# Kernel tuning notes

Measured on AMD Instinct MI355X. Metric: run time of the kernel, lower is better.

The kernel has to match this reference:

```python
import jax, jax.numpy as jnp
import numpy as np

D = 1024
POOL_SIZES = [1024, 512, 256, 128, 64]  # n_pos=32*32 -> n_codes=64
CODEBOOK_SIZE = 512
BATCH = 32
W_SCALE = 0.03125  # ~1/sqrt(D) so pre-softmax logits stay O(1)


def setup_inputs() -> dict:
    key = jax.random.key(0)
    ks = jax.random.split(key, 7)
    x = jax.random.normal(ks[0], (BATCH, POOL_SIZES[0], D), dtype=jnp.float32)
    queries = jax.random.normal(ks[1], (len(POOL_SIZES), POOL_SIZES[0], D), dtype=jnp.float32)
    wq = jax.random.normal(ks[2], (len(POOL_SIZES), D, D), dtype=jnp.float32) * W_SCALE
    wk = jax.random.normal(ks[3], (len(POOL_SIZES), D, D), dtype=jnp.float32) * W_SCALE
    wv = jax.random.normal(ks[4], (len(POOL_SIZES), D, D), dtype=jnp.float32) * W_SCALE
    wo = jax.random.normal(ks[5], (len(POOL_SIZES), D, D), dtype=jnp.float32) * W_SCALE
    codebook = jax.random.normal(ks[6], (CODEBOOK_SIZE, D), dtype=jnp.float32)
    return {"x": x, "queries": queries, "wq": wq, "wk": wk, "wv": wv, "wo": wo, "codebook": codebook}


def reference(x, queries, wq, wk, wv, wo, codebook):
    # StackedPooling: S -> 1024 -> 512 -> 256 -> 128 -> 64 via AttentionPool stages
    scale = D ** (-0.5)
    h = x
    for i, K in enumerate(POOL_SIZES):
        q = queries[i, :K, :] @ wq[i]              # [K, D] learned queries, q_proj
        k = jnp.einsum("bsd,de->bse", h, wk[i])    # [B, S, D]
        v = jnp.einsum("bsd,de->bse", h, wv[i])    # [B, S, D]
        logits = jnp.einsum("kd,bsd->bks", q, k) * scale
        attn = jax.nn.softmax(logits, axis=-1)     # [B, K, S]
        pooled = jnp.einsum("bks,bsd->bkd", attn, v)
        h = jnp.einsum("bkd,de->bke", pooled, wo[i])  # [B, K, D]
    # VQ codebook quantization: nearest code per latent (squared L2)
    z = h                                          # [B, n_codes, D]
    d2 = (jnp.sum(z * z, axis=-1, keepdims=True)
          - 2.0 * jnp.einsum("bkd,cd->bkc", z, codebook)
          + jnp.sum(codebook * codebook, axis=-1))  # [B, n_codes, C]
    idx = jnp.argmin(d2, axis=-1)                  # [B, n_codes] int
    z_q = codebook[idx]                            # [B, n_codes, D]
    # straight-through estimator
    out = z + jax.lax.stop_gradient(z_q - z)
    return out
```

## Files before the change

### kernel.cpp

```cpp
#include <hip/hip_runtime.h>


#define MB (1024ull * 1024ull)

typedef unsigned short u16;
typedef __attribute__((ext_vector_type(4))) float f32x4;
typedef __bf16 bf16x8 __attribute__((ext_vector_type(8)));

__device__ __forceinline__ u16 f2bf(float f) {
  unsigned u = __float_as_uint(f);
  unsigned r = u + 0x7FFFu + ((u >> 16) & 1u);
  return (u16)(r >> 16);
}
__device__ __forceinline__ float bf2f(u16 h) {
  return __uint_as_float(((unsigned)h) << 16);
}

typedef __attribute__((address_space(1))) const void GASV;
typedef __attribute__((address_space(3))) void LASV;
__device__ __forceinline__ void async16(const void* g, void* l) {
  __builtin_amdgcn_global_load_lds((GASV*)g, (LASV*)l, 16, 0, 0);
}

__device__ __forceinline__ int xcd_swz(int bid, int nwg) {
  const int q8 = nwg >> 3, r8 = nwg & 7;
  const int xcd = bid & 7, idx = bid >> 3;
  return (xcd < r8 ? xcd * (q8 + 1) : r8 * (q8 + 1) + (xcd - r8) * q8) + idx;
}

template<int MODE>
__global__ __launch_bounds__(512, 1)
void gemm_c(const u16* __restrict__ A, const u16* __restrict__ B,
            float* __restrict__ Cf, u16* __restrict__ Cb,
            int M, int N, int KLEN, int ld,
            long long sA, long long sB, long long sC, int ldc, float alpha,
            int nxt, int nyt)
{
  __shared__ u16 lds[65536];
  const int tid  = threadIdx.x;
  const int lane = tid & 63;
  const int w    = tid >> 6;
  const int wr   = w >> 2, wc = w & 3;

  const int wg = xcd_swz((int)blockIdx.x, (int)gridDim.x);
  const int bx = wg % nxt;
  const int by = (wg / nxt) % nyt;
  const int bz = wg / (nxt * nyt);

  const int m0 = by * 256, n0 = bx * 256;
  const u16* Ab = A + (size_t)bz * sA;
  const u16* Bb = B + (size_t)bz * sB;
  const int NT = KLEN >> 6;

  f32x4 acc[8][4] = {};

  const int Rl  = tid >> 2;
  const int sgs = (tid & 3) ^ ((tid >> 3) & 3);
  int ra0 = m0 + Rl;        ra0 = ra0 < M - 1 ? ra0 : M - 1;
  int ra1 = m0 + 128 + Rl;  ra1 = ra1 < M - 1 ? ra1 : M - 1;
  int rb0 = n0 + Rl;        rb0 = rb0 < N - 1 ? rb0 : N - 1;
  int rb1 = n0 + 128 + Rl;  rb1 = rb1 < N - 1 ? rb1 : N - 1;
  const u16* gA0 = Ab + (size_t)ra0 * ld + (sgs << 3);
  const u16* gA1 = Ab + (size_t)ra1 * ld + (sgs << 3);
  const u16* gB0 = Bb + (size_t)rb0 * ld + (sgs << 3);
  const u16* gB1 = Bb + (size_t)rb1 * ld + (sgs << 3);
  const int ldst = (w << 4) * 32;

  auto stageH = [&](int mat, int buf, int kh, int tile) {
    const int tt = tile < NT ? tile : NT - 1;
    const int kc = (tt << 6) + (kh << 5);
    u16* d = &lds[(mat << 15) + (buf << 14) + (kh << 13) + ldst];
    if (mat == 0) { async16(gA0 + kc, d); async16(gA1 + kc, d + 4096); }
    else          { async16(gB0 + kc, d); async16(gB1 + kc, d + 4096); }
  };

  const int rsel = lane & 15;
  const int ksub = lane >> 4;
  const int sw   = ksub ^ ((rsel >> 1) & 3);
  const u16* ldsA = &lds[(wr * 128 + rsel) * 32 + sw * 8];
  const u16* ldsB = &lds[32768 + (wc * 64 + rsel) * 32 + sw * 8];

  auto phase = [&](int buf, int kh, int mh, bf16x8* b,
                   int smat, int sbuf, int skh, int stile, int vm) {
    bf16x8 a[4];
    if (mh == 0) {
#pragma unroll
      for (int ni = 0; ni < 4; ++ni)
        b[ni] = *(const bf16x8*)&ldsB[buf * 16384 + kh * 8192 + ni * 512];
    }
#pragma unroll
    for (int mi = 0; mi < 4; ++mi)
      a[mi] = *(const bf16x8*)&ldsA[buf * 16384 + kh * 8192 + mh * 2048 + mi * 512];
    stageH(smat, sbuf, skh, stile);
    if (vm == 10)     asm volatile("s_waitcnt vmcnt(10)" ::: "memory");
    else if (vm == 6) asm volatile("s_waitcnt vmcnt(6)" ::: "memory");
    __builtin_amdgcn_s_barrier();
    asm volatile("s_waitcnt lgkmcnt(0)" ::: "memory");
    __builtin_amdgcn_sched_barrier(0);
    __builtin_amdgcn_s_setprio(1);
#pragma unroll
    for (int mi = 0; mi < 4; ++mi)
#pragma unroll
      for (int ni = 0; ni < 4; ++ni)
        acc[mh * 4 + mi][ni] = __builtin_amdgcn_mfma_f32_16x16x32_bf16(
            a[mi], b[ni], acc[mh * 4 + mi][ni], 0, 0, 0);
    __builtin_amdgcn_s_setprio(0);
    __builtin_amdgcn_s_barrier();
  };

  stageH(1, 0, 0, 0); stageH(0, 0, 0, 0); stageH(1, 0, 1, 0); stageH(0, 0, 1, 0);
  stageH(1, 1, 0, 1); stageH(0, 1, 0, 1); stageH(1, 1, 1, 1);
  asm volatile("s_waitcnt vmcnt(6)" ::: "memory");
  __builtin_amdgcn_s_barrier();

  const int NI = NT >> 1;
  for (int it = 0; it < NI; ++it) {
    const int t0 = it << 1, t1 = t0 + 1;
    bf16x8 b0[4], b1[4];
    phase(0, 0, 0, b0, 0, 1, 1, t1,     -1);
    phase(0, 0, 1, b0, 1, 0, 0, t0 + 2, -1);
    phase(0, 1, 0, b1, 0, 0, 0, t0 + 2, -1);
    phase(0, 1, 1, b1, 1, 0, 1, t0 + 2, 10);
    phase(1, 0, 0, b0, 0, 0, 1, t0 + 2, -1);
    phase(1, 0, 1, b0, 1, 1, 0, t1 + 2, 10);
    phase(1, 1, 0, b1, 0, 1, 0, t1 + 2, -1);
    phase(1, 1, 1, b1, 1, 1, 1, t1 + 2, 6);
  }
  asm volatile("s_waitcnt vmcnt(0)" ::: "memory");

#pragma unroll
  for (int mi = 0; mi < 8; ++mi)
#pragma unroll
    for (int ni = 0; ni < 4; ++ni)
#pragma unroll
      for (int i = 0; i < 4; ++i) {
        const int row = m0 + wr * 128 + mi * 16 + ((lane >> 4) << 2) + i;
        const int col = n0 + wc * 64 + ni * 16 + rsel;
        if (row < M && col < N) {
          const float v = acc[mi][ni][i] * alpha;
          const size_t off = (size_t)bz * sC + (size_t)row * ldc + col;
          if (MODE == 0) Cf[off] = v;
          else           Cb[off] = f2bf(v);
        }
      }
}

template<int MODE>
__global__ __launch_bounds__(256, 2)
void gemm_s(const u16* __restrict__ A, const u16* __restrict__ B,
            float* __restrict__ Cf, u16* __restrict__ Cb,
            int M, int N, int KLEN, int ld,
            long long sA, long long sB, long long sC, int ldc, float alpha,
            int nxt, int nyt)
{
  __shared__ u16 lds[32768];
  const int tid  = threadIdx.x;
  const int lane = tid & 63;
  const int w    = tid >> 6;
  const int wr   = w >> 1, wc = w & 1;

  const int wg = xcd_swz((int)blockIdx.x, (int)gridDim.x);
  const int bx = wg % nxt;
  const int by = (wg / nxt) % nyt;
  const int bz = wg / (nxt * nyt);

  const int m0 = by * 128, n0 = bx * 128;
  const u16* Ab = A + (size_t)bz * sA;
  const u16* Bb = B + (size_t)bz * sB;
  const int NT = KLEN >> 6;

  f32x4 acc[4][4] = {};

  const int Rl  = tid >> 3;
  const int sgs = (tid & 7) ^ (Rl & 7);
  const int ldst = (w << 3) * 64;

  auto stage = [&](int t, int buf) {
    const int kc = t << 6;
#pragma unroll
    for (int mat = 0; mat < 2; ++mat)
#pragma unroll
      for (int j = 0; j < 4; ++j) {
        int rg = (mat ? n0 : m0) + j * 32 + Rl;
        const int lim = (mat ? N : M) - 1;
        rg = rg < lim ? rg : lim;
        const u16* src = (mat ? Bb : Ab) + (size_t)rg * ld + kc + (sgs << 3);
        async16(src, &lds[(buf << 14) + (mat << 13) + j * 2048 + ldst]);
      }
  };

  const int rsel = lane & 15, ksub = lane >> 4;
  const int e  = rsel & 7;
  const int s0 = ((e >> 2) << 2) | (ksub ^ (e & 3));
  const int s1 = s0 ^ 4;
  const u16* ldsA0 = &lds[(wr * 64 + rsel) * 64 + s0 * 8];
  const u16* ldsA1 = &lds[(wr * 64 + rsel) * 64 + s1 * 8];
  const u16* ldsB0 = &lds[8192 + (wc * 64 + rsel) * 64 + s0 * 8];
  const u16* ldsB1 = &lds[8192 + (wc * 64 + rsel) * 64 + s1 * 8];

  stage(0, 0);
  for (int t = 0; t < NT; ++t) {
    const int buf = t & 1;
    if (t + 1 < NT) {
      stage(t + 1, buf ^ 1);
      asm volatile("s_waitcnt vmcnt(8)" ::: "memory");
    } else {
      asm volatile("s_waitcnt vmcnt(0)" ::: "memory");
    }
    __builtin_amdgcn_s_barrier();
    bf16x8 af[4][2], bf[4][2];
#pragma unroll
    for (int f = 0; f < 4; ++f) {
      af[f][0] = *(const bf16x8*)&ldsA0[buf * 16384 + f * 1024];
      af[f][1] = *(const bf16x8*)&ldsA1[buf * 16384 + f * 1024];
      bf[f][0] = *(const bf16x8*)&ldsB0[buf * 16384 + f * 1024];
      bf[f][1] = *(const bf16x8*)&ldsB1[buf * 16384 + f * 1024];
    }
    asm volatile("s_waitcnt lgkmcnt(0)" ::: "memory");
    __builtin_amdgcn_sched_barrier(0);
    __builtin_amdgcn_s_setprio(1);
#pragma unroll
    for (int mi = 0; mi < 4; ++mi)
#pragma unroll
      for (int ni = 0; ni < 4; ++ni)
#pragma unroll
        for (int kh = 0; kh < 2; ++kh)
          acc[mi][ni] = __builtin_amdgcn_mfma_f32_16x16x32_bf16(
              af[mi][kh], bf[ni][kh], acc[mi][ni], 0, 0, 0);
    __builtin_amdgcn_s_setprio(0);
    __builtin_amdgcn_s_barrier();
  }

#pragma unroll
  for (int mi = 0; mi < 4; ++mi)
#pragma unroll
    for (int ni = 0; ni < 4; ++ni)
#pragma unroll
      for (int i = 0; i < 4; ++i) {
        const int row = m0 + wr * 64 + mi * 16 + ((lane >> 4) << 2) + i;
        const int col = n0 + wc * 64 + ni * 16 + rsel;
        if (row < M && col < N) {
          const float v = acc[mi][ni][i] * alpha;
          const size_t off = (size_t)bz * sC + (size_t)row * ldc + col;
          if (MODE == 0) Cf[off] = v;
          else           Cb[off] = f2bf(v);
        }
      }
}

__global__ void cast_k(const float* __restrict__ in, u16* __restrict__ out,
                       long long n4)
{
  long long i = (long long)blockIdx.x * 256 + threadIdx.x;
  const long long stride = (long long)gridDim.x * 256;
  for (; i < n4; i += stride) {
    const float4 v = *(const float4*)&in[i << 2];
    *(ushort4*)&out[i << 2] = make_ushort4(f2bf(v.x), f2bf(v.y), f2bf(v.z), f2bf(v.w));
  }
}

__global__ __launch_bounds__(256)
void cast_trans_k(const float* __restrict__ in, u16* __restrict__ h,
                  u16* __restrict__ ht)
{
  __shared__ float t[32][33];
  const int z = blockIdx.z;
  const float* src = in + (size_t)z * 1048576;
  u16* dh = h  + (size_t)z * 1048576;
  u16* dt = ht + (size_t)z * 1048576;
  const int x0 = blockIdx.x * 32, y0 = blockIdx.y * 32;
  const int tx = threadIdx.x, ty = threadIdx.y;
#pragma unroll
  for (int k = 0; k < 4; ++k) {
    const float v = src[(size_t)(y0 + ty + 8 * k) * 1024 + (x0 + tx)];
    t[ty + 8 * k][tx] = v;
    dh[(size_t)(y0 + ty + 8 * k) * 1024 + (x0 + tx)] = f2bf(v);
  }
  __syncthreads();
#pragma unroll
  for (int k = 0; k < 4; ++k)
    dt[(size_t)(x0 + ty + 8 * k) * 1024 + (y0 + tx)] = f2bf(t[tx][ty + 8 * k]);
}

__global__ __launch_bounds__(256)
void transpose_cast_k(const float* __restrict__ in, u16* __restrict__ out)
{
  __shared__ float t[32][33];
  const int z = blockIdx.z;
  const float* src = in + (size_t)z * 1048576;
  u16* dst = out + (size_t)z * 1048576;
  const int x0 = blockIdx.x * 32, y0 = blockIdx.y * 32;
  const int tx = threadIdx.x, ty = threadIdx.y;
#pragma unroll
  for (int k = 0; k < 4; ++k)
    t[ty + 8 * k][tx] = src[(size_t)(y0 + ty + 8 * k) * 1024 + (x0 + tx)];
  __syncthreads();
#pragma unroll
  for (int k = 0; k < 4; ++k)
    dst[(size_t)(x0 + ty + 8 * k) * 1024 + (y0 + tx)] = f2bf(t[tx][ty + 8 * k]);
}

__global__ __launch_bounds__(256)
void transpose_u16_k(const u16* __restrict__ in, u16* __restrict__ out, int R)
{
  __shared__ u16 t[32][33];
  const size_t zi = (size_t)blockIdx.z * R * 1024;
  const size_t zo = (size_t)blockIdx.z * 1024 * R;
  const int x0 = blockIdx.x * 32, y0 = blockIdx.y * 32;
  const int tx = threadIdx.x, ty = threadIdx.y;
#pragma unroll
  for (int k = 0; k < 4; ++k)
    t[ty + 8 * k][tx] = in[zi + (size_t)(y0 + ty + 8 * k) * 1024 + (x0 + tx)];
  __syncthreads();
#pragma unroll
  for (int k = 0; k < 4; ++k)
    out[zo + (size_t)(x0 + ty + 8 * k) * R + (y0 + tx)] = t[tx][ty + 8 * k];
}

__global__ __launch_bounds__(256)
void softmax_b(const u16* __restrict__ lg, u16* __restrict__ at, int S)
{
  const size_t row = blockIdx.x;
  const u16* src = lg + row * S;
  const int tid = threadIdx.x;
  float v[4];
  float mx = -3.402823466e38f;
#pragma unroll
  for (int c = 0; c < 4; ++c) {
    const int j = tid + c * 256;
    v[c] = (j < S) ? bf2f(src[j]) : -3.402823466e38f;
    mx = fmaxf(mx, v[c]);
  }
#pragma unroll
  for (int o = 32; o > 0; o >>= 1) mx = fmaxf(mx, __shfl_xor(mx, o));
  __shared__ float rmx[4];
  if ((tid & 63) == 0) rmx[tid >> 6] = mx;
  __syncthreads();
  mx = fmaxf(fmaxf(rmx[0], rmx[1]), fmaxf(rmx[2], rmx[3]));
  float sum = 0.f;
#pragma unroll
  for (int c = 0; c < 4; ++c) { v[c] = expf(v[c] - mx); sum += v[c]; }
#pragma unroll
  for (int o = 32; o > 0; o >>= 1) sum += __shfl_xor(sum, o);
  __shared__ float rsm[4];
  if ((tid & 63) == 0) rsm[tid >> 6] = sum;
  __syncthreads();
  sum = rsm[0] + rsm[1] + rsm[2] + rsm[3];
  const float inv = 1.0f / sum;
  u16* dst = at + row * S;
#pragma unroll
  for (int c = 0; c < 4; ++c) {
    const int j = tid + c * 256;
    if (j < S) dst[j] = f2bf(v[c] * inv);
  }
}

__global__ __launch_bounds__(256)
void cnorm_kernel(const float* __restrict__ cb, float* __restrict__ cn)
{
  const int c = blockIdx.x;
  const float4 v = ((const float4*)(cb + (size_t)c * 1024))[threadIdx.x];
  float s = v.x * v.x + v.y * v.y + v.z * v.z + v.w * v.w;
#pragma unroll
  for (int o = 32; o > 0; o >>= 1) s += __shfl_xor(s, o);
  __shared__ float r4[4];
  if ((threadIdx.x & 63) == 0) r4[threadIdx.x >> 6] = s;
  __syncthreads();
  if (threadIdx.x == 0) cn[c] = r4[0] + r4[1] + r4[2] + r4[3];
}

__global__ __launch_bounds__(256)
void argmin_gather_k(const float* __restrict__ dot, const float* __restrict__ cn,
                     const float* __restrict__ cb, float* __restrict__ out)
{
  const size_t lat = blockIdx.x;
  const int tid = threadIdx.x;
  const float* dr = dot + lat * 512;
  float best = 3.402823466e38f;
  int bi = 0;
#pragma unroll
  for (int cc = 0; cc < 2; ++cc) {
    const int c = tid + cc * 256;
    const float sc = cn[c] - 2.0f * dr[c];
    if (sc < best || (sc == best && c < bi)) { best = sc; bi = c; }
  }
  __shared__ float rb[256];
  __shared__ int   ri[256];
  rb[tid] = best; ri[tid] = bi;
  __syncthreads();
  for (int s = 128; s > 0; s >>= 1) {
    if (tid < s) {
      const float ob = rb[tid + s];
      const int oi = ri[tid + s];
      if (ob < rb[tid] || (ob == rb[tid] && oi < ri[tid])) { rb[tid] = ob; ri[tid] = oi; }
    }
    __syncthreads();
  }
  const int sel = ri[0];
  ((float4*)(out + lat * 1024))[tid] = ((const float4*)(cb + (size_t)sel * 1024))[tid];
}

__global__ void fill_kernel(float* p, float v, int n) {
  const int i = blockIdx.x * 256 + threadIdx.x;
  if (i < n) p[i] = v;
}

static void gX(hipStream_t st, int mode, int force,
               const u16* A, const u16* B, float* Cf, u16* Cb,
               int M, int N, int KLEN, int ld,
               long long sA, long long sB, long long sC, int ldc,
               int batch, float alpha)
{
  const int b256 = ((M + 255) / 256) * ((N + 255) / 256) * batch;
  const bool big = (force == 2) || (force == 0 && b256 >= 192 && (KLEN & 127) == 0);
  if (big) {
    const int nxt = (N + 255) / 256, nyt = (M + 255) / 256;
    dim3 grid(nxt * nyt * batch), blk(512);
    if (mode == 0)
      gemm_c<0><<<grid, blk, 0, st>>>(A, B, Cf, Cb, M, N, KLEN, ld, sA, sB, sC, ldc, alpha, nxt, nyt);
    else
      gemm_c<1><<<grid, blk, 0, st>>>(A, B, Cf, Cb, M, N, KLEN, ld, sA, sB, sC, ldc, alpha, nxt, nyt);
  } else {
    const int nxt = (N + 127) / 128, nyt = (M + 127) / 128;
    dim3 grid(nxt * nyt * batch), blk(256);
    if (mode == 0)
      gemm_s<0><<<grid, blk, 0, st>>>(A, B, Cf, Cb, M, N, KLEN, ld, sA, sB, sC, ldc, alpha, nxt, nyt);
    else
      gemm_s<1><<<grid, blk, 0, st>>>(A, B, Cf, Cb, M, N, KLEN, ld, sA, sB, sC, ldc, alpha, nxt, nyt);
  }
}

extern "C" void kernel_launch(void* const* d_in, const int* in_sizes, int n_in,
                              void* d_out, int out_size, void* d_ws, size_t ws_size,
                              hipStream_t stream)
{
  const float* x   = (const float*)d_in[0];
  const float* qry = (const float*)d_in[1];
  const float* wq  = (const float*)d_in[2];
  const float* wk  = (const float*)d_in[3];
  const float* wv  = (const float*)d_in[4];
  const float* wo  = (const float*)d_in[5];
  const float* cb  = (const float*)d_in[6];
  float* out = (float*)d_out;

  const size_t NEED = 312 * MB;
  if (ws_size < NEED) {
    fill_kernel<<<(out_size + 255) / 256, 256, 0, stream>>>(out, (float)ws_size, out_size);
    return;
  }
  char* ws = (char*)d_ws;
  const long long W = 1048576;
  u16*  QKb  = (u16*)(ws + 0 * MB);
  u16*  WVOb = (u16*)(ws + 10 * MB);
  u16*  WVOs = (u16*)(ws + 20 * MB);
  u16*  CBb  = (u16*)(ws + 30 * MB);
  float* CN  = (float*)(ws + 31 * MB);
  u16*  QKP  = (u16*)(ws + 32 * MB);
  u16*  WCb  = (u16*)(ws + 40 * MB);
  u16*  WC5  = (u16*)(ws + 48 * MB);
  u16*  CBW  = (u16*)(ws + 50 * MB);
  float* DOT = (float*)(ws + 51 * MB);
  u16*  U    = (u16*)(ws + 56 * MB);
  u16*  UT   = (u16*)(ws + 120 * MB);
  u16*  ATb  = (u16*)(ws + 184 * MB);
  u16*  LOG  = (u16*)(ws + 248 * MB);
  u16*  QSb   = (u16*)(ws + 56 * MB);
  u16*  WQb   = (u16*)(ws + 66 * MB);
  u16*  WKb   = (u16*)(ws + 76 * MB);
  u16*  WVb   = (u16*)(ws + 86 * MB);
  u16*  WOTb  = (u16*)(ws + 96 * MB);
  u16*  WqkTb = (u16*)(ws + 106 * MB);

  const int S_in[5]  = {1024, 1024, 512, 256, 128};
  const int K_out[5] = {1024, 512, 256, 128, 64};

  cast_k<<<2048, 256, 0, stream>>>(qry, QSb, 1310720ll);
  cast_k<<<2048, 256, 0, stream>>>(wq, WQb, 1310720ll);
  cast_k<<<2048, 256, 0, stream>>>(wk, WKb, 1310720ll);
  cast_k<<<2048, 256, 0, stream>>>(wv, WVb, 1310720ll);
  cast_k<<<512, 256, 0, stream>>>(cb, CBb, 131072ll);
  dim3 tb(32, 8), tg5(32, 32, 5);
  transpose_cast_k<<<tg5, tb, 0, stream>>>(wo, WOTb);
  cnorm_kernel<<<512, 256, 0, stream>>>(cb, CN);

  gX(stream, 1, 0, WKb, WQb, nullptr, WqkTb, 1024, 1024, 1024, 1024, W, W, W, 1024, 5, 1.0f);
  gX(stream, 1, 0, QSb, WqkTb, nullptr, QKb, 1024, 1024, 1024, 1024, W, W, W, 1024, 5, 1.0f);
  gX(stream, 1, 0, WOTb, WVb, nullptr, WVOb, 1024, 1024, 1024, 1024, W, W, W, 1024, 5, 1.0f);
  gX(stream, 1, 0, WVb, WOTb, nullptr, WVOs, 1024, 1024, 1024, 1024, W, W, W, 1024, 5, 1.0f);

  hipMemcpyAsync(WCb, WVOs, 2 * MB, hipMemcpyDeviceToDevice, stream);
  gX(stream, 1, 0, WCb,         WVOb + 1 * W, nullptr, WCb + 1 * W, 1024, 1024, 1024, 1024, 0, 0, 0, 1024, 1, 1.0f);
  gX(stream, 1, 0, WCb + 1 * W, WVOb + 2 * W, nullptr, WCb + 2 * W, 1024, 1024, 1024, 1024, 0, 0, 0, 1024, 1, 1.0f);
  gX(stream, 1, 0, WCb + 2 * W, WVOb + 3 * W, nullptr, WCb + 3 * W, 1024, 1024, 1024, 1024, 0, 0, 0, 1024, 1, 1.0f);
  gX(stream, 1, 0, WCb + 3 * W, WVOb + 4 * W, nullptr, WC5,         1024, 1024, 1024, 1024, 0, 0, 0, 1024, 1, 1.0f);
  gX(stream, 1, 0, QKb + W, WCb, nullptr, QKP, 1024, 1024, 1024, 1024, W, W, W, 1024, 4, 1.0f);
  gX(stream, 1, 0, CBb, WC5, nullptr, CBW, 512, 1024, 1024, 1024, 0, 0, 0, 1024, 1, 1.0f);

  dim3 tgx(32, 32, 32);
  cast_trans_k<<<tgx, tb, 0, stream>>>(x, U, UT);

  for (int i = 0; i < 5; ++i) {
    const int S = S_in[i], KO = K_out[i];
    const u16* qk = (i == 0) ? QKb : QKP + (size_t)(i - 1) * W;

    gX(stream, 1, (i == 0) ? 1 : 0, qk, U, nullptr, LOG,
       KO, S, 1024, 1024, 0, (long long)S * 1024, (long long)KO * S, S, 32, 0.03125f);
    softmax_b<<<32 * KO, 256, 0, stream>>>(LOG, ATb, S);
    gX(stream, 1, (i == 0) ? 2 : 0, ATb, UT, nullptr, U,
       KO, 1024, S, S, (long long)KO * S, (long long)1024 * S, (long long)KO * 1024, 1024, 32, 1.0f);
    if (i < 4) {
      dim3 tgt(32, KO / 32, 32);
      transpose_u16_k<<<tgt, tb, 0, stream>>>(U, UT, KO);
    }
  }

  gX(stream, 0, 0, U, CBW, DOT, nullptr,
     2048, 512, 1024, 1024, 0, 0, 0, 512, 1, 1.0f);
  argmin_gather_k<<<2048, 256, 0, stream>>>(DOT, CN, cb, out);
}
```

Before: 733.1 us.

## Fuse transposed output into GEMM epilogue, merge cast kernels, batch weight products

Adds a GEMM mode that writes a transposed bf16 copy of the pooled output from the epilogue, replacing the separate transpose kernel between stages. The transposed buffer ping-pongs between two workspace regions. The five cast launches are merged into one kernel. The WK·WQ and WV·WOT products now run as a single batch of 10, and the memcpy is replaced by a transpose. The forced big/small GEMM tile selection is dropped. The transposed epilogue stores are strided and uncoalesced, which may cost more than the transpose kernel they replace.

```diff
diff --git a/kernel.cpp b/kernel.cpp
--- a/kernel.cpp
+++ b/kernel.cpp
@@ -31,10 +31,10 @@
 template<int MODE>
 __global__ __launch_bounds__(512, 1)
 void gemm_c(const u16* __restrict__ A, const u16* __restrict__ B,
-            float* __restrict__ Cf, u16* __restrict__ Cb,
+            float* __restrict__ Cf, u16* __restrict__ Cb, u16* __restrict__ Ct,
             int M, int N, int KLEN, int ld,
-            long long sA, long long sB, long long sC, int ldc, float alpha,
-            int nxt, int nyt)
+            long long sA, long long sB, long long sC, int ldc,
+            long long sT, int ldt, float alpha, int nxt, int nyt)
 {
   __shared__ u16 lds[65536];
   const int tid  = threadIdx.x;
@@ -140,7 +140,12 @@
           const float v = acc[mi][ni][i] * alpha;
           const size_t off = (size_t)bz * sC + (size_t)row * ldc + col;
           if (MODE == 0) Cf[off] = v;
-          else           Cb[off] = f2bf(v);
+          else {
+            const u16 h = f2bf(v);
+            Cb[off] = h;
+            if (MODE == 2)
+              Ct[(size_t)bz * sT + (size_t)col * ldt + row] = h;
+          }
         }
       }
 }
@@ -148,10 +153,10 @@
 template<int MODE>
 __global__ __launch_bounds__(256, 2)
 void gemm_s(const u16* __restrict__ A, const u16* __restrict__ B,
-            float* __restrict__ Cf, u16* __restrict__ Cb,
+            float* __restrict__ Cf, u16* __restrict__ Cb, u16* __restrict__ Ct,
             int M, int N, int KLEN, int ld,
-            long long sA, long long sB, long long sC, int ldc, float alpha,
-            int nxt, int nyt)
+            long long sA, long long sB, long long sC, int ldc,
+            long long sT, int ldt, float alpha, int nxt, int nyt)
 {
   __shared__ u16 lds[32768];
   const int tid  = threadIdx.x;
@@ -243,19 +248,34 @@
           const float v = acc[mi][ni][i] * alpha;
           const size_t off = (size_t)bz * sC + (size_t)row * ldc + col;
           if (MODE == 0) Cf[off] = v;
-          else           Cb[off] = f2bf(v);
+          else {
+            const u16 h = f2bf(v);
+            Cb[off] = h;
+            if (MODE == 2)
+              Ct[(size_t)bz * sT + (size_t)col * ldt + row] = h;
+          }
         }
       }
 }
 
-__global__ void cast_k(const float* __restrict__ in, u16* __restrict__ out,
-                       long long n4)
+__global__ void multicast_k(const float* __restrict__ q, const float* __restrict__ wqp,
+                            const float* __restrict__ wkp, const float* __restrict__ wvp,
+                            const float* __restrict__ cbp,
+                            u16* __restrict__ dq, u16* __restrict__ dwq,
+                            u16* __restrict__ dwk, u16* __restrict__ dwv,
+                            u16* __restrict__ dcb)
 {
   long long i = (long long)blockIdx.x * 256 + threadIdx.x;
   const long long stride = (long long)gridDim.x * 256;
-  for (; i < n4; i += stride) {
-    const float4 v = *(const float4*)&in[i << 2];
-    *(ushort4*)&out[i << 2] = make_ushort4(f2bf(v.x), f2bf(v.y), f2bf(v.z), f2bf(v.w));
+  for (; i < 5373952ll; i += stride) {
+    const float* src; u16* dst; long long j;
+    if (i < 1310720)      { src = q;   dst = dq;  j = i; }
+    else if (i < 2621440) { src = wqp; dst = dwq; j = i - 1310720; }
+    else if (i < 3932160) { src = wkp; dst = dwk; j = i - 2621440; }
+    else if (i < 5242880) { src = wvp; dst = dwv; j = i - 3932160; }
+    else                  { src = cbp; dst = dcb; j = i - 5242880; }
+    const float4 v = *(const float4*)&src[j << 2];
+    *(ushort4*)&dst[j << 2] = make_ushort4(f2bf(v.x), f2bf(v.y), f2bf(v.z), f2bf(v.w));
   }
 }
 
@@ -405,28 +425,31 @@
   if (i < n) p[i] = v;
 }
 
-static void gX(hipStream_t st, int mode, int force,
-               const u16* A, const u16* B, float* Cf, u16* Cb,
+static void gX(hipStream_t st, int mode,
+               const u16* A, const u16* B, float* Cf, u16* Cb, u16* Ct,
                int M, int N, int KLEN, int ld,
                long long sA, long long sB, long long sC, int ldc,
-               int batch, float alpha)
+               long long sT, int ldt, int batch, float alpha)
 {
   const int b256 = ((M + 255) / 256) * ((N + 255) / 256) * batch;
-  const bool big = (force == 2) || (force == 0 && b256 >= 192 && (KLEN & 127) == 0);
-  if (big) {
+  if (b256 >= 192 && (KLEN & 127) == 0) {
     const int nxt = (N + 255) / 256, nyt = (M + 255) / 256;
     dim3 grid(nxt * nyt * batch), blk(512);
     if (mode == 0)
-      gemm_c<0><<<grid, blk, 0, st>>>(A, B, Cf, Cb, M, N, KLEN, ld, sA, sB, sC, ldc, alpha, nxt, nyt);
+      gemm_c<0><<<grid, blk, 0, st>>>(A, B, Cf, Cb, Ct, M, N, KLEN, ld, sA, sB, sC, ldc, sT, ldt, alpha, nxt, nyt);
+    else if (mode == 1)
+      gemm_c<1><<<grid, blk, 0, st>>>(A, B, Cf, Cb, Ct, M, N, KLEN, ld, sA, sB, sC, ldc, sT, ldt, alpha, nxt, nyt);
     else
-      gemm_c<1><<<grid, blk, 0, st>>>(A, B, Cf, Cb, M, N, KLEN, ld, sA, sB, sC, ldc, alpha, nxt, nyt);
+      gemm_c<2><<<grid, blk, 0, st>>>(A, B, Cf, Cb, Ct, M, N, KLEN, ld, sA, sB, sC, ldc, sT, ldt, alpha, nxt, nyt);
   } else {
     const int nxt = (N + 127) / 128, nyt = (M + 127) / 128;
     dim3 grid(nxt * nyt * batch), blk(256);
     if (mode == 0)
-      gemm_s<0><<<grid, blk, 0, st>>>(A, B, Cf, Cb, M, N, KLEN, ld, sA, sB, sC, ldc, alpha, nxt, nyt);
+      gemm_s<0><<<grid, blk, 0, st>>>(A, B, Cf, Cb, Ct, M, N, KLEN, ld, sA, sB, sC, ldc, sT, ldt, alpha, nxt, nyt);
+    else if (mode == 1)
+      gemm_s<1><<<grid, blk, 0, st>>>(A, B, Cf, Cb, Ct, M, N, KLEN, ld, sA, sB, sC, ldc, sT, ldt, alpha, nxt, nyt);
     else
-      gemm_s<1><<<grid, blk, 0, st>>>(A, B, Cf, Cb, M, N, KLEN, ld, sA, sB, sC, ldc, alpha, nxt, nyt);
+      gemm_s<2><<<grid, blk, 0, st>>>(A, B, Cf, Cb, Ct, M, N, KLEN, ld, sA, sB, sC, ldc, sT, ldt, alpha, nxt, nyt);
   }
 }
 
@@ -443,78 +466,79 @@
   const float* cb  = (const float*)d_in[6];
   float* out = (float*)d_out;
 
-  const size_t NEED = 312 * MB;
+  const size_t NEED = 376 * MB;
   if (ws_size < NEED) {
     fill_kernel<<<(out_size + 255) / 256, 256, 0, stream>>>(out, (float)ws_size, out_size);
     return;
   }
   char* ws = (char*)d_ws;
   const long long W = 1048576;
-  u16*  QKb  = (u16*)(ws + 0 * MB);
-  u16*  WVOb = (u16*)(ws + 10 * MB);
-  u16*  WVOs = (u16*)(ws + 20 * MB);
-  u16*  CBb  = (u16*)(ws + 30 * MB);
-  float* CN  = (float*)(ws + 31 * MB);
-  u16*  QKP  = (u16*)(ws + 32 * MB);
-  u16*  WCb  = (u16*)(ws + 40 * MB);
-  u16*  WC5  = (u16*)(ws + 48 * MB);
-  u16*  CBW  = (u16*)(ws + 50 * MB);
-  float* DOT = (float*)(ws + 51 * MB);
+  u16*  QKb   = (u16*)(ws + 0 * MB);
+  u16*  WqkTb = (u16*)(ws + 10 * MB);
+  u16*  WVOb  = (u16*)(ws + 20 * MB);
+  u16*  CBb   = (u16*)(ws + 30 * MB);
+  float* CN   = (float*)(ws + 31 * MB);
+  u16*  QKP   = (u16*)(ws + 32 * MB);
+  u16*  WCb   = (u16*)(ws + 40 * MB);
+  u16*  WC5   = (u16*)(ws + 48 * MB);
+  u16*  CBW   = (u16*)(ws + 50 * MB);
+  float* DOT  = (float*)(ws + 51 * MB);
   u16*  U    = (u16*)(ws + 56 * MB);
-  u16*  UT   = (u16*)(ws + 120 * MB);
+  u16*  UTa  = (u16*)(ws + 120 * MB);
   u16*  ATb  = (u16*)(ws + 184 * MB);
   u16*  LOG  = (u16*)(ws + 248 * MB);
-  u16*  QSb   = (u16*)(ws + 56 * MB);
-  u16*  WQb   = (u16*)(ws + 66 * MB);
-  u16*  WKb   = (u16*)(ws + 76 * MB);
-  u16*  WVb   = (u16*)(ws + 86 * MB);
-  u16*  WOTb  = (u16*)(ws + 96 * MB);
-  u16*  WqkTb = (u16*)(ws + 106 * MB);
+  u16*  UTb2 = (u16*)(ws + 312 * MB);
+  u16*  QSb  = (u16*)(ws + 56 * MB);
+  u16*  WQb  = (u16*)(ws + 66 * MB);
+  u16*  WVb  = (u16*)(ws + 76 * MB);
+  u16*  WKb  = (u16*)(ws + 86 * MB);
+  u16*  WOTb = (u16*)(ws + 96 * MB);
 
   const int S_in[5]  = {1024, 1024, 512, 256, 128};
   const int K_out[5] = {1024, 512, 256, 128, 64};
 
-  cast_k<<<2048, 256, 0, stream>>>(qry, QSb, 1310720ll);
-  cast_k<<<2048, 256, 0, stream>>>(wq, WQb, 1310720ll);
-  cast_k<<<2048, 256, 0, stream>>>(wk, WKb, 1310720ll);
-  cast_k<<<2048, 256, 0, stream>>>(wv, WVb, 1310720ll);
-  cast_k<<<512, 256, 0, stream>>>(cb, CBb, 131072ll);
+  multicast_k<<<2048, 256, 0, stream>>>(qry, wq, wk, wv, cb,
+                                        QSb, WQb, WKb, WVb, CBb);
   dim3 tb(32, 8), tg5(32, 32, 5);
   transpose_cast_k<<<tg5, tb, 0, stream>>>(wo, WOTb);
   cnorm_kernel<<<512, 256, 0, stream>>>(cb, CN);
 
-  gX(stream, 1, 0, WKb, WQb, nullptr, WqkTb, 1024, 1024, 1024, 1024, W, W, W, 1024, 5, 1.0f);
-  gX(stream, 1, 0, QSb, WqkTb, nullptr, QKb, 1024, 1024, 1024, 1024, W, W, W, 1024, 5, 1.0f);
-  gX(stream, 1, 0, WOTb, WVb, nullptr, WVOb, 1024, 1024, 1024, 1024, W, W, W, 1024, 5, 1.0f);
-  gX(stream, 1, 0, WVb, WOTb, nullptr, WVOs, 1024, 1024, 1024, 1024, W, W, W, 1024, 5, 1.0f);
-
-  hipMemcpyAsync(WCb, WVOs, 2 * MB, hipMemcpyDeviceToDevice, stream);
-  gX(stream, 1, 0, WCb,         WVOb + 1 * W, nullptr, WCb + 1 * W, 1024, 1024, 1024, 1024, 0, 0, 0, 1024, 1, 1.0f);
-  gX(stream, 1, 0, WCb + 1 * W, WVOb + 2 * W, nullptr, WCb + 2 * W, 1024, 1024, 1024, 1024, 0, 0, 0, 1024, 1, 1.0f);
-  gX(stream, 1, 0, WCb + 2 * W, WVOb + 3 * W, nullptr, WCb + 3 * W, 1024, 1024, 1024, 1024, 0, 0, 0, 1024, 1, 1.0f);
-  gX(stream, 1, 0, WCb + 3 * W, WVOb + 4 * W, nullptr, WC5,         1024, 1024, 1024, 1024, 0, 0, 0, 1024, 1, 1.0f);
-  gX(stream, 1, 0, QKb + W, WCb, nullptr, QKP, 1024, 1024, 1024, 1024, W, W, W, 1024, 4, 1.0f);
-  gX(stream, 1, 0, CBb, WC5, nullptr, CBW, 512, 1024, 1024, 1024, 0, 0, 0, 1024, 1, 1.0f);
+  gX(stream, 1, WKb, WQb, nullptr, WqkTb, nullptr,
+     1024, 1024, 1024, 1024, W, W, W, 1024, 0, 0, 10, 1.0f);
+  gX(stream, 1, QSb, WqkTb, nullptr, QKb, nullptr,
+     1024, 1024, 1024, 1024, W, W, W, 1024, 0, 0, 5, 1.0f);
+
+  {
+    dim3 tgt(32, 32, 1);
+    transpose_u16_k<<<tgt, tb, 0, stream>>>(WVOb, WCb, 1024);
+  }
+  gX(stream, 1, WCb,         WVOb + 1 * W, nullptr, WCb + 1 * W, nullptr, 1024, 1024, 1024, 1024, 0, 0, 0, 1024, 0, 0, 1, 1.0f);
+  gX(stream, 1, WCb + 1 * W, WVOb + 2 * W, nullptr, WCb + 2 * W, nullptr, 1024, 1024, 1024, 1024, 0, 0, 0, 1024, 0, 0, 1, 1.0f);
+  gX(stream, 1, WCb + 2 * W, WVOb + 3 * W, nullptr, WCb + 3 * W, nullptr, 1024, 1024, 1024, 1024, 0, 0, 0, 1024, 0, 0, 1, 1.0f);
+  gX(stream, 1, WCb + 3 * W, WVOb + 4 * W, nullptr, WC5,         nullptr, 1024, 1024, 1024, 1024, 0, 0, 0, 1024, 0, 0, 1, 1.0f);
+  gX(stream, 1, QKb + W, WCb, nullptr, QKP, nullptr,
+     1024, 1024, 1024, 1024, W, W, W, 1024, 0, 0, 4, 1.0f);
+  gX(stream, 1, CBb, WC5, nullptr, CBW, nullptr,
+     512, 1024, 1024, 1024, 0, 0, 0, 1024, 0, 0, 1, 1.0f);
 
   dim3 tgx(32, 32, 32);
-  cast_trans_k<<<tgx, tb, 0, stream>>>(x, U, UT);
+  cast_trans_k<<<tgx, tb, 0, stream>>>(x, U, UTa);
 
   for (int i = 0; i < 5; ++i) {
     const int S = S_in[i], KO = K_out[i];
     const u16* qk = (i == 0) ? QKb : QKP + (size_t)(i - 1) * W;
-
-    gX(stream, 1, (i == 0) ? 1 : 0, qk, U, nullptr, LOG,
-       KO, S, 1024, 1024, 0, (long long)S * 1024, (long long)KO * S, S, 32, 0.03125f);
+    const u16* utin  = (i & 1) ? UTb2 : UTa;
+    u16*       utout = (i & 1) ? UTa  : UTb2;
+
+    gX(stream, 1, qk, U, nullptr, LOG, nullptr,
+       KO, S, 1024, 1024, 0, (long long)S * 1024, (long long)KO * S, S, 0, 0, 32, 0.03125f);
     softmax_b<<<32 * KO, 256, 0, stream>>>(LOG, ATb, S);
-    gX(stream, 1, (i == 0) ? 2 : 0, ATb, UT, nullptr, U,
-       KO, 1024, S, S, (long long)KO * S, (long long)1024 * S, (long long)KO * 1024, 1024, 32, 1.0f);
-    if (i < 4) {
-      dim3 tgt(32, KO / 32, 32);
-      transpose_u16_k<<<tgt, tb, 0, stream>>>(U, UT, KO);
-    }
-  }
-
-  gX(stream, 0, 0, U, CBW, DOT, nullptr,
-     2048, 512, 1024, 1024, 0, 0, 0, 512, 1, 1.0f);
+    gX(stream, (i < 4) ? 2 : 1, ATb, utin, nullptr, U, utout,
+       KO, 1024, S, S, (long long)KO * S, (long long)1024 * S,
+       (long long)KO * 1024, 1024, (long long)1024 * KO, KO, 32, 1.0f);
+  }
+
+  gX(stream, 0, U, CBW, DOT, nullptr, nullptr,
+     2048, 512, 1024, 1024, 0, 0, 0, 512, 0, 0, 1, 1.0f);
   argmin_gather_k<<<2048, 256, 0, stream>>>(DOT, CN, cb, out);
 }
```

Result: no change. 746.6 us (+1.8%).
